# Kernel optimization log

Measured on AMD Instinct MI355X. Metric: run time of the kernel, lower is better.

The kernel has to match this reference:

```python
import jax, jax.numpy as jnp
import numpy as np

N_HEADS = 16
HEAD_DIM = 64  # dim=1024 / n_heads=16


def setup_inputs() -> dict:
    key = jax.random.key(0)
    ks = jax.random.split(key, 7)
    B, S, D = 4, 2048, 1024
    scale = 1.0 / np.sqrt(D)
    return {
        "q": jax.random.normal(ks[0], (B, S, D), jnp.float32),
        "k": jax.random.normal(ks[1], (B, S, D), jnp.float32),
        "v": jax.random.normal(ks[2], (B, S, D), jnp.float32),
        "Wq": jax.random.normal(ks[3], (D, D), jnp.float32) * scale,
        "Wk": jax.random.normal(ks[4], (D, D), jnp.float32) * scale,
        "Wv": jax.random.normal(ks[5], (D, D), jnp.float32) * scale,
        "Wo": jax.random.normal(ks[6], (D, D), jnp.float32) * scale,
    }


def reference(q, k, v, Wq, Wk, Wv, Wo):
    B, S, _ = q.shape
    H, Dh = N_HEADS, HEAD_DIM
    # linear projections (torch Linear: x @ W.T), reshape to [B, H, S, Dh]
    xq = (q @ Wq.T).reshape(B, S, H, Dh).transpose(0, 2, 1, 3)
    xk = (k @ Wk.T).reshape(B, S, H, Dh).transpose(0, 2, 1, 3)
    xv = (v @ Wv.T).reshape(B, S, H, Dh).transpose(0, 2, 1, 3)
    scores = jnp.einsum("bhsd,bhtd->bhst", xq, xk) / jnp.sqrt(jnp.float32(Dh))
    # causal mask: -inf above diagonal
    causal = jnp.triu(jnp.full((S, S), -jnp.inf, jnp.float32), k=1)
    scores = scores + causal[None, None]
    attn = jax.nn.softmax(scores.astype(jnp.float32), axis=-1).astype(xq.dtype)
    out = jnp.einsum("bhst,bhtd->bhsd", attn, xv)
    out = out.transpose(0, 2, 1, 3).reshape(B, S, H * Dh)
    return out @ Wo.T
```

## Files before the change

kernel.cpp:

```cpp
#include <hip/hip_runtime.h>
#include <hip/hip_bf16.h>

#define DI __device__ __forceinline__

typedef __attribute__((ext_vector_type(8))) short short8;
typedef __attribute__((ext_vector_type(4))) short short4v;
typedef __attribute__((ext_vector_type(4))) float f32x4;

#define QSCALE 0.180336885f

DI short f2bf(float f) {
  unsigned u = __builtin_bit_cast(unsigned, f);
  unsigned r = u + 0x7fffu + ((u >> 16) & 1u);
  return (short)(r >> 16);
}

DI unsigned cvt_pk(float lo, float hi) {
  unsigned r;
  asm("v_cvt_pk_bf16_f32 %0, %1, %2" : "=v"(r) : "v"(lo), "v"(hi));
  return r;
}

DI float fexp2(float x) {
#if __has_builtin(__builtin_amdgcn_exp2f)
  return __builtin_amdgcn_exp2f(x);
#else
  return exp2f(x);
#endif
}

DI void gl16(const short* g, short* l) {
  __builtin_amdgcn_global_load_lds(
      (const __attribute__((address_space(1))) void*)g,
      (__attribute__((address_space(3))) void*)l, 16, 0, 0);
}

__global__ __launch_bounds__(256) void convert_w(
    const float* __restrict__ wq, const float* __restrict__ wk,
    const float* __restrict__ wv, const float* __restrict__ wo,
    short* __restrict__ dst) {
  int z = blockIdx.z;
  const float* src = (z == 0) ? wq : (z == 1) ? wk : (z == 2) ? wv : wo;
  short* d = dst + (size_t)z * 1024 * 1024;
  int i = (blockIdx.x * 256 + threadIdx.x) * 4;
  float4 f = *(const float4*)(src + i);
  short4v v;
  v[0] = f2bf(f.x); v[1] = f2bf(f.y); v[2] = f2bf(f.z); v[3] = f2bf(f.w);
  *(short4v*)(d + i) = v;
}

__global__ __launch_bounds__(256) void convert_x(
    const float* __restrict__ q, const float* __restrict__ k,
    const float* __restrict__ v, short* __restrict__ qb,
    short* __restrict__ kb, short* __restrict__ vb) {
  int z = blockIdx.z;
  const float* src = (z == 0) ? q : (z == 1) ? k : v;
  short* dst = (z == 0) ? qb : (z == 1) ? kb : vb;
  size_t i = ((size_t)blockIdx.x * 256 + threadIdx.x) * 8;
  float4 f0 = *(const float4*)(src + i);
  float4 f1 = *(const float4*)(src + i + 4);
  short8 o;
  o[0] = f2bf(f0.x); o[1] = f2bf(f0.y); o[2] = f2bf(f0.z); o[3] = f2bf(f0.w);
  o[4] = f2bf(f1.x); o[5] = f2bf(f1.y); o[6] = f2bf(f1.z); o[7] = f2bf(f1.w);
  *(short8*)(dst + i) = o;
}

__global__ __launch_bounds__(256) void convert_one(
    const float* __restrict__ src, short* __restrict__ dst) {
  size_t i = ((size_t)blockIdx.x * 256 + threadIdx.x) * 8;
  float4 f0 = *(const float4*)(src + i);
  float4 f1 = *(const float4*)(src + i + 4);
  short8 o;
  o[0] = f2bf(f0.x); o[1] = f2bf(f0.y); o[2] = f2bf(f0.z); o[3] = f2bf(f0.w);
  o[4] = f2bf(f1.x); o[5] = f2bf(f1.y); o[6] = f2bf(f1.z); o[7] = f2bf(f1.w);
  *(short8*)(dst + i) = o;
}

enum { OUT_F32 = 0, OUT_HEAD = 1, OUT_HEADT = 2 };

template <int OMODE>
DI void gemm_core(const short* __restrict__ A, const short* __restrict__ B,
                  void* __restrict__ Cp, float scale, int bm, int bn) {
  __shared__ __align__(16) short sA[128 * 64];
  __shared__ __align__(16) short sB[128 * 64];

  const int tid = threadIdx.x;
  const int lane = tid & 63;
  const int wid = tid >> 6;
  const int wm = wid >> 1, wn = wid & 1;
  const int l15 = lane & 15, lq = lane >> 4;
  const int lrr = lane >> 3;
  const int lch = lane & 7;

  f32x4 acc[4][4] = {};

  for (int k0 = 0; k0 < 1024; k0 += 64) {
#pragma unroll
    for (int i = 0; i < 4; ++i) {
      int r0 = wid * 32 + i * 8;
      int rr = r0 + lrr;
      int sc = (lch ^ (rr & 7)) << 3;
      gl16(A + (size_t)(bm + rr) * 1024 + k0 + sc, sA + r0 * 64);
      gl16(B + (size_t)(bn + rr) * 1024 + k0 + sc, sB + r0 * 64);
    }
    __syncthreads();

#pragma unroll
    for (int ks = 0; ks < 2; ++ks) {
      short8 a[4], b[4];
#pragma unroll
      for (int mt = 0; mt < 4; ++mt) {
        int row = wm * 64 + mt * 16 + l15;
        int off = (row * 128 + ks * 64 + lq * 16) ^ ((row & 7) << 4);
        a[mt] = *(const short8*)((const char*)sA + off);
      }
#pragma unroll
      for (int nt = 0; nt < 4; ++nt) {
        int row = wn * 64 + nt * 16 + l15;
        int off = (row * 128 + ks * 64 + lq * 16) ^ ((row & 7) << 4);
        b[nt] = *(const short8*)((const char*)sB + off);
      }
#pragma unroll
      for (int mt = 0; mt < 4; ++mt)
#pragma unroll
        for (int nt = 0; nt < 4; ++nt) {
          if (OMODE == OUT_HEADT)
            acc[mt][nt] = __builtin_amdgcn_mfma_f32_16x16x32_bf16(
                b[nt], a[mt], acc[mt][nt], 0, 0, 0);
          else
            acc[mt][nt] = __builtin_amdgcn_mfma_f32_16x16x32_bf16(
                a[mt], b[nt], acc[mt][nt], 0, 0, 0);
        }
    }
    __syncthreads();
  }

#pragma unroll
  for (int mt = 0; mt < 4; ++mt) {
#pragma unroll
    for (int nt = 0; nt < 4; ++nt) {
#pragma unroll
      for (int r = 0; r < 4; ++r) {
        float val = acc[mt][nt][r] * scale;
        if (OMODE == OUT_HEADT) {
          int f = bn + wn * 64 + nt * 16 + lq * 4 + r;
          int t = bm + wm * 64 + mt * 16 + l15;
          int bb = t >> 11, s = t & 2047;
          int h = f >> 6, dh = f & 63;
          ((short*)Cp)[((size_t)((bb * 16 + h) * 64 + dh)) * 2048 + s] = f2bf(val);
        } else {
          int rowg = bm + wm * 64 + mt * 16 + lq * 4 + r;
          int colg = bn + wn * 64 + nt * 16 + l15;
          if (OMODE == OUT_HEAD) {
            int bb = rowg >> 11, s = rowg & 2047;
            int h = colg >> 6, dh = colg & 63;
            ((short*)Cp)[((size_t)(bb * 16 + h) * 2048 + s) * 64 + dh] = f2bf(val);
          } else {
            ((float*)Cp)[(size_t)rowg * 1024 + colg] = val;
          }
        }
      }
    }
  }
}

DI void xcd_map(int id, int& bm, int& bn) {
  int xcd = id & 7, slot = id >> 3;
  int panel = xcd + 8 * (slot >> 3);
  int ntile = slot & 7;
  bm = panel * 128;
  bn = ntile * 128;
}

__global__ __launch_bounds__(256) void proj_gemm3(
    const short* __restrict__ qb, const short* __restrict__ kb,
    const short* __restrict__ vb, const short* __restrict__ wq,
    const short* __restrict__ wk, const short* __restrict__ wv,
    short* __restrict__ xq, short* __restrict__ xk, short* __restrict__ xvT) {
  int z = blockIdx.z;
  int bm, bn;
  xcd_map(blockIdx.x, bm, bn);
  if (z == 0) {
    gemm_core<OUT_HEAD>(qb, wq, xq, QSCALE, bm, bn);
  } else if (z == 1) {
    gemm_core<OUT_HEAD>(kb, wk, xk, 1.0f, bm, bn);
  } else {
    gemm_core<OUT_HEADT>(vb, wv, xvT, 1.0f, bm, bn);
  }
}

__global__ __launch_bounds__(256) void proj_oneN(
    const short* __restrict__ A, const short* __restrict__ B,
    short* __restrict__ C, float scale) {
  int bm, bn;
  xcd_map(blockIdx.x, bm, bn);
  gemm_core<OUT_HEAD>(A, B, C, scale, bm, bn);
}

__global__ __launch_bounds__(256) void proj_oneT(
    const short* __restrict__ A, const short* __restrict__ B,
    short* __restrict__ C, float scale) {
  int bm, bn;
  xcd_map(blockIdx.x, bm, bn);
  gemm_core<OUT_HEADT>(A, B, C, scale, bm, bn);
}

__global__ __launch_bounds__(256) void final_gemm(
    const short* __restrict__ oa, const short* __restrict__ wo,
    float* __restrict__ out) {
  int bm, bn;
  xcd_map(blockIdx.x, bm, bn);
  gemm_core<OUT_F32>(oa, wo, out, 1.0f, bm, bn);
}

__global__ __launch_bounds__(256) void attn_k(
    const short* __restrict__ Xq, const short* __restrict__ Xk,
    const short* __restrict__ XvT, short* __restrict__ Oa) {
  __shared__ __align__(16) short sK[64 * 64];
  __shared__ __align__(16) short sVT[64 * 64];
  __shared__ __align__(16) short sP[4][16 * 64];

  const int tid = threadIdx.x;
  const int lane = tid & 63;
  const int wid = tid >> 6;
  const int l15 = lane & 15, lq = lane >> 4;
  const int bid = blockIdx.x;
  const int ipair = bid >> 6;
  const int bh = bid & 63;
  const int b = bh >> 4, h = bh & 15;

  const short* Q = Xq + (size_t)bh * 2048 * 64;
  const short* K = Xk + (size_t)bh * 2048 * 64;
  const short* VT = XvT + (size_t)bh * 64 * 2048;

  const int srow = tid >> 3;
  const int scol = (tid & 7) * 8;
  const int soff0 = (srow * 128 + scol * 2) ^ ((srow & 7) << 4);
  const int soff1 = ((srow + 32) * 128 + scol * 2) ^ ((srow & 7) << 4);

  short8 kreg[2], vreg[2];
  kreg[0] = *(const short8*)(K + (size_t)srow * 64 + scol);
  kreg[1] = *(const short8*)(K + (size_t)(srow + 32) * 64 + scol);
  vreg[0] = *(const short8*)(VT + (size_t)srow * 2048 + scol);
  vreg[1] = *(const short8*)(VT + (size_t)(srow + 32) * 2048 + scol);

  short* sPw = sP[wid];

  for (int seg = 0; seg < 2; ++seg) {
    const int qt = seg ? ipair : (31 - ipair);
    const int qrow0 = qt * 64 + wid * 16;
    const int qg = qrow0 + l15;

    short8 qf[2];
#pragma unroll
    for (int ks = 0; ks < 2; ++ks)
      qf[ks] = *(const short8*)(Q + (size_t)qg * 64 + ks * 32 + lq * 8);

    float m_run = -1e30f, l_run = 0.f;
    f32x4 acc[4] = {};

    for (int kt = 0; kt <= qt; ++kt) {
      const int kv0 = kt * 64;
      *(short8*)((char*)sK + soff0) = kreg[0];
      *(short8*)((char*)sK + soff1) = kreg[1];
      *(short8*)((char*)sVT + soff0) = vreg[0];
      *(short8*)((char*)sVT + soff1) = vreg[1];
      __syncthreads();

      {
        int nkt = kt + 1, nseg = seg;
        if (nkt > qt) { nseg = seg + 1; nkt = 0; }
        if (nseg < 2) {
          const int kn = nkt * 64;
          kreg[0] = *(const short8*)(K + (size_t)(kn + srow) * 64 + scol);
          kreg[1] = *(const short8*)(K + (size_t)(kn + srow + 32) * 64 + scol);
          vreg[0] = *(const short8*)(VT + (size_t)srow * 2048 + kn + scol);
          vreg[1] = *(const short8*)(VT + (size_t)(srow + 32) * 2048 + kn + scol);
        }
      }

      f32x4 sc[4] = {};
      __builtin_amdgcn_s_setprio(1);
#pragma unroll
      for (int ks = 0; ks < 2; ++ks) {
        short8 kf[4];
#pragma unroll
        for (int nt = 0; nt < 4; ++nt) {
          int row = nt * 16 + l15;
          int off = (row * 128 + ks * 64 + lq * 16) ^ ((row & 7) << 4);
          kf[nt] = *(const short8*)((const char*)sK + off);
        }
#pragma unroll
        for (int nt = 0; nt < 4; ++nt)
          sc[nt] = __builtin_amdgcn_mfma_f32_16x16x32_bf16(kf[nt], qf[ks], sc[nt], 0, 0, 0);
      }
      __builtin_amdgcn_s_setprio(0);

      float p[4][4];
      float m = -1e30f;
      const bool diag = (kt == qt);
#pragma unroll
      for (int nt = 0; nt < 4; ++nt) {
#pragma unroll
        for (int r = 0; r < 4; ++r) {
          float s = sc[nt][r];
          if (diag && (kv0 + nt * 16 + lq * 4 + r > qg)) s = -1e30f;
          p[nt][r] = s;
          m = fmaxf(m, s);
        }
      }
      m = fmaxf(m, __shfl_xor(m, 16));
      m = fmaxf(m, __shfl_xor(m, 32));

      if (!__all(m - m_run <= 8.0f)) {
        const float m_new = fmaxf(m_run, m);
        const float corr = fexp2(m_run - m_new);
        l_run *= corr;
#pragma unroll
        for (int mt = 0; mt < 4; ++mt)
#pragma unroll
          for (int r = 0; r < 4; ++r) acc[mt][r] *= corr;
        m_run = m_new;
      }

      float rsum = 0.f;
#pragma unroll
      for (int nt = 0; nt < 4; ++nt)
#pragma unroll
        for (int r = 0; r < 4; ++r) {
          float e = fexp2(p[nt][r] - m_run);
          p[nt][r] = e;
          rsum += e;
        }
      rsum += __shfl_xor(rsum, 16);
      rsum += __shfl_xor(rsum, 32);
      l_run += rsum;

#pragma unroll
      for (int nt = 0; nt < 4; ++nt) {
        uint2 pw;
        pw.x = cvt_pk(p[nt][0], p[nt][1]);
        pw.y = cvt_pk(p[nt][2], p[nt][3]);
        int off = (l15 * 128 + nt * 32 + lq * 8) ^ ((l15 & 7) << 4);
        *(uint2*)((char*)sPw + off) = pw;
      }

      __builtin_amdgcn_s_setprio(1);
#pragma unroll
      for (int ks = 0; ks < 2; ++ks) {
        int poff = (l15 * 128 + ks * 64 + lq * 16) ^ ((l15 & 7) << 4);
        short8 pf = *(const short8*)((const char*)sPw + poff);
#pragma unroll
        for (int mt = 0; mt < 4; ++mt) {
          int row = mt * 16 + l15;
          int voff = (row * 128 + ks * 64 + lq * 16) ^ ((row & 7) << 4);
          short8 vf = *(const short8*)((const char*)sVT + voff);
          acc[mt] = __builtin_amdgcn_mfma_f32_16x16x32_bf16(vf, pf, acc[mt], 0, 0, 0);
        }
      }
      __builtin_amdgcn_s_setprio(0);
      __syncthreads();
    }

    const float rl = 1.0f / l_run;
    short* orow = Oa + ((size_t)(b * 2048 + qg)) * 1024 + h * 64;
#pragma unroll
    for (int mt = 0; mt < 4; ++mt) {
      uint2 o;
      o.x = cvt_pk(acc[mt][0] * rl, acc[mt][1] * rl);
      o.y = cvt_pk(acc[mt][2] * rl, acc[mt][3] * rl);
      *(uint2*)(orow + mt * 16 + lq * 4) = o;
    }
  }
}

extern "C" void kernel_launch(void* const* d_in, const int* in_sizes, int n_in,
                              void* d_out, int out_size, void* d_ws,
                              size_t ws_size, hipStream_t stream) {
  const float* q = (const float*)d_in[0];
  const float* k = (const float*)d_in[1];
  const float* v = (const float*)d_in[2];
  const float* Wq = (const float*)d_in[3];
  const float* Wk = (const float*)d_in[4];
  const float* Wv = (const float*)d_in[5];
  const float* Wo = (const float*)d_in[6];

  char* ws = (char*)d_ws;
  short* wq_b = (short*)(ws + (0ull << 20));
  short* wk_b = (short*)(ws + (2ull << 20));
  short* wv_b = (short*)(ws + (4ull << 20));
  short* wo_b = (short*)(ws + (6ull << 20));
  short* xq  = (short*)(ws + (8ull << 20));
  short* xk  = (short*)(ws + (24ull << 20));
  short* xvT = (short*)(ws + (56ull << 20));

  convert_w<<<dim3(1024, 1, 4), 256, 0, stream>>>(Wq, Wk, Wv, Wo, wq_b);

  if (ws_size >= (122ull << 20)) {
    short* qb = (short*)(ws + (72ull << 20));
    short* kb = (short*)(ws + (88ull << 20));
    short* vb = (short*)(ws + (104ull << 20));
    short* oa = qb;

    convert_x<<<dim3(4096, 1, 3), 256, 0, stream>>>(q, k, v, qb, kb, vb);
    proj_gemm3<<<dim3(512, 1, 3), 256, 0, stream>>>(qb, kb, vb, wq_b, wk_b,
                                                    wv_b, xq, xk, xvT);
    attn_k<<<dim3(1024), 256, 0, stream>>>(xq, xk, xvT, oa);
    final_gemm<<<dim3(512), 256, 0, stream>>>(oa, wo_b, (float*)d_out);
  } else {
    short* X = (short*)(ws + (8ull << 20));
    short* xq2 = (short*)(ws + (24ull << 20));
    short* xk2 = (short*)(ws + (40ull << 20));
    short* xvT2 = (short*)(ws + (56ull << 20));
    short* oa2 = (short*)(ws + (72ull << 20));

    convert_one<<<dim3(4096), 256, 0, stream>>>(q, X);
    proj_oneN<<<dim3(512), 256, 0, stream>>>(X, wq_b, xq2, QSCALE);
    convert_one<<<dim3(4096), 256, 0, stream>>>(k, X);
    proj_oneN<<<dim3(512), 256, 0, stream>>>(X, wk_b, xk2, 1.0f);
    convert_one<<<dim3(4096), 256, 0, stream>>>(v, X);
    proj_oneT<<<dim3(512), 256, 0, stream>>>(X, wv_b, xvT2, 1.0f);
    attn_k<<<dim3(1024), 256, 0, stream>>>(xq2, xk2, xvT2, oa2);
    final_gemm<<<dim3(512), 256, 0, stream>>>(oa2, wo_b, (float*)d_out);
  }
}
```

Before: 197.8 us.

## Double-buffer K/V tiles in attention LDS and drop one barrier per tile

The attention kernel now keeps two LDS buffers for K and V^T. The next tile is stored into the alternate buffer after the current tile's MFMAs, which leaves one __syncthreads per iteration instead of two. It also sets a minimum of 4 blocks per CU in launch_bounds, and replaces the inline-asm packed bf16 convert with a software round-to-nearest-even conversion. In exchange, LDS use rises and the software conversion costs more ALU instructions, which may offset the gain from the removed barrier.

```diff
diff --git a/kernel.cpp b/kernel.cpp
--- a/kernel.cpp
+++ b/kernel.cpp
@@ -13,12 +13,6 @@
   unsigned u = __builtin_bit_cast(unsigned, f);
   unsigned r = u + 0x7fffu + ((u >> 16) & 1u);
   return (short)(r >> 16);
-}
-
-DI unsigned cvt_pk(float lo, float hi) {
-  unsigned r;
-  asm("v_cvt_pk_bf16_f32 %0, %1, %2" : "=v"(r) : "v"(lo), "v"(hi));
-  return r;
 }
 
 DI float fexp2(float x) {
@@ -213,11 +207,11 @@
   gemm_core<OUT_F32>(oa, wo, out, 1.0f, bm, bn);
 }
 
-__global__ __launch_bounds__(256) void attn_k(
+__global__ __launch_bounds__(256, 4) void attn_k(
     const short* __restrict__ Xq, const short* __restrict__ Xk,
     const short* __restrict__ XvT, short* __restrict__ Oa) {
-  __shared__ __align__(16) short sK[64 * 64];
-  __shared__ __align__(16) short sVT[64 * 64];
+  __shared__ __align__(16) short sK[2][64 * 64];
+  __shared__ __align__(16) short sVT[2][64 * 64];
   __shared__ __align__(16) short sP[4][16 * 64];
 
   const int tid = threadIdx.x;
@@ -244,7 +238,13 @@
   vreg[0] = *(const short8*)(VT + (size_t)srow * 2048 + scol);
   vreg[1] = *(const short8*)(VT + (size_t)(srow + 32) * 2048 + scol);
 
+  *(short8*)((char*)sK[0] + soff0) = kreg[0];
+  *(short8*)((char*)sK[0] + soff1) = kreg[1];
+  *(short8*)((char*)sVT[0] + soff0) = vreg[0];
+  *(short8*)((char*)sVT[0] + soff1) = vreg[1];
+
   short* sPw = sP[wid];
+  int p = 0;
 
   for (int seg = 0; seg < 2; ++seg) {
     const int qt = seg ? ipair : (31 - ipair);
@@ -261,23 +261,21 @@
 
     for (int kt = 0; kt <= qt; ++kt) {
       const int kv0 = kt * 64;
-      *(short8*)((char*)sK + soff0) = kreg[0];
-      *(short8*)((char*)sK + soff1) = kreg[1];
-      *(short8*)((char*)sVT + soff0) = vreg[0];
-      *(short8*)((char*)sVT + soff1) = vreg[1];
       __syncthreads();
 
-      {
-        int nkt = kt + 1, nseg = seg;
-        if (nkt > qt) { nseg = seg + 1; nkt = 0; }
-        if (nseg < 2) {
-          const int kn = nkt * 64;
-          kreg[0] = *(const short8*)(K + (size_t)(kn + srow) * 64 + scol);
-          kreg[1] = *(const short8*)(K + (size_t)(kn + srow + 32) * 64 + scol);
-          vreg[0] = *(const short8*)(VT + (size_t)srow * 2048 + kn + scol);
-          vreg[1] = *(const short8*)(VT + (size_t)(srow + 32) * 2048 + kn + scol);
-        }
-      }
+      int nkt = kt + 1, nseg = seg;
+      if (nkt > qt) { nseg = seg + 1; nkt = 0; }
+      const bool hn = (nseg < 2);
+      if (hn) {
+        const int kn = nkt * 64;
+        kreg[0] = *(const short8*)(K + (size_t)(kn + srow) * 64 + scol);
+        kreg[1] = *(const short8*)(K + (size_t)(kn + srow + 32) * 64 + scol);
+        vreg[0] = *(const short8*)(VT + (size_t)srow * 2048 + kn + scol);
+        vreg[1] = *(const short8*)(VT + (size_t)(srow + 32) * 2048 + kn + scol);
+      }
+
+      const char* bufK = (const char*)sK[p];
+      const char* bufV = (const char*)sVT[p];
 
       f32x4 sc[4] = {};
       __builtin_amdgcn_s_setprio(1);
@@ -288,7 +286,7 @@
         for (int nt = 0; nt < 4; ++nt) {
           int row = nt * 16 + l15;
           int off = (row * 128 + ks * 64 + lq * 16) ^ ((row & 7) << 4);
-          kf[nt] = *(const short8*)((const char*)sK + off);
+          kf[nt] = *(const short8*)(bufK + off);
         }
 #pragma unroll
         for (int nt = 0; nt < 4; ++nt)
@@ -296,7 +294,7 @@
       }
       __builtin_amdgcn_s_setprio(0);
 
-      float p[4][4];
+      float pv[4][4];
       float m = -1e30f;
       const bool diag = (kt == qt);
 #pragma unroll
@@ -305,7 +303,7 @@
         for (int r = 0; r < 4; ++r) {
           float s = sc[nt][r];
           if (diag && (kv0 + nt * 16 + lq * 4 + r > qg)) s = -1e30f;
-          p[nt][r] = s;
+          pv[nt][r] = s;
           m = fmaxf(m, s);
         }
       }
@@ -328,8 +326,8 @@
       for (int nt = 0; nt < 4; ++nt)
 #pragma unroll
         for (int r = 0; r < 4; ++r) {
-          float e = fexp2(p[nt][r] - m_run);
-          p[nt][r] = e;
+          float e = fexp2(pv[nt][r] - m_run);
+          pv[nt][r] = e;
           rsum += e;
         }
       rsum += __shfl_xor(rsum, 16);
@@ -338,11 +336,11 @@
 
 #pragma unroll
       for (int nt = 0; nt < 4; ++nt) {
-        uint2 pw;
-        pw.x = cvt_pk(p[nt][0], p[nt][1]);
-        pw.y = cvt_pk(p[nt][2], p[nt][3]);
+        short4v pw;
+#pragma unroll
+        for (int r = 0; r < 4; ++r) pw[r] = f2bf(pv[nt][r]);
         int off = (l15 * 128 + nt * 32 + lq * 8) ^ ((l15 & 7) << 4);
-        *(uint2*)((char*)sPw + off) = pw;
+        *(short4v*)((char*)sPw + off) = pw;
       }
 
       __builtin_amdgcn_s_setprio(1);
@@ -354,22 +352,29 @@
         for (int mt = 0; mt < 4; ++mt) {
           int row = mt * 16 + l15;
           int voff = (row * 128 + ks * 64 + lq * 16) ^ ((row & 7) << 4);
-          short8 vf = *(const short8*)((const char*)sVT + voff);
+          short8 vf = *(const short8*)(bufV + voff);
           acc[mt] = __builtin_amdgcn_mfma_f32_16x16x32_bf16(vf, pf, acc[mt], 0, 0, 0);
         }
       }
       __builtin_amdgcn_s_setprio(0);
-      __syncthreads();
+
+      if (hn) {
+        *(short8*)((char*)sK[p ^ 1] + soff0) = kreg[0];
+        *(short8*)((char*)sK[p ^ 1] + soff1) = kreg[1];
+        *(short8*)((char*)sVT[p ^ 1] + soff0) = vreg[0];
+        *(short8*)((char*)sVT[p ^ 1] + soff1) = vreg[1];
+      }
+      p ^= 1;
     }
 
     const float rl = 1.0f / l_run;
     short* orow = Oa + ((size_t)(b * 2048 + qg)) * 1024 + h * 64;
 #pragma unroll
     for (int mt = 0; mt < 4; ++mt) {
-      uint2 o;
-      o.x = cvt_pk(acc[mt][0] * rl, acc[mt][1] * rl);
-      o.y = cvt_pk(acc[mt][2] * rl, acc[mt][3] * rl);
-      *(uint2*)(orow + mt * 16 + lq * 4) = o;
+      short4v o;
+#pragma unroll
+      for (int r = 0; r < 4; ++r) o[r] = f2bf(acc[mt][r] * rl);
+      *(short4v*)(orow + mt * 16 + lq * 4) = o;
     }
   }
 }
```

Measured after the change: 184.6 us. -6.7%, faster.
